# Performance work log

Measured on AMD Instinct MI355X. Metric: run time of the kernel, lower is better.

## Reference

```python
import jax, jax.numpy as jnp
import numpy as np

T = 16          # time_span
N = 128         # num_trajectory
D = 512         # embedding dim
TEMP = 0.1      # temperature
INF = 1000000000.0
M = 2 * N * T   # total rows of z (two views)


def setup_inputs() -> dict:
    key = jax.random.key(0)
    k1, k2 = jax.random.split(key)
    z = jax.random.normal(k1, (M, D), dtype=jnp.float32)
    done = jax.random.randint(k2, (T, N), 0, 2).astype(jnp.int32)  # [T, N] binary done flags
    return {"z": z, "done": done}


def _build_positive_mask(done):
    # done: [T, N] int -> transposed to [N, T] as in the torch code
    d = done.astype(jnp.float32).T  # [N, T]
    # Sequential rewrite loop is equivalent to:
    #   done_new[r,t] = 1 iff exists original done at p < t in row r AND orig done[r,t] == 0
    excl = jnp.cumsum(d, axis=1) - d  # exclusive cumsum along time
    d_new = jnp.where((excl > 0) & (d == 0), 1.0, 0.0)  # [N, T]
    done_vec = 1.0 - d_new.reshape(-1)  # [N*T]
    # block-diagonal temporal mask: same trajectory => 1
    traj = jnp.arange(N * T) // T
    block = (traj[:, None] == traj[None, :]).astype(jnp.float32)  # [NT, NT]
    done_mask = (done_vec[:, None] * done_vec[None, :]) * block
    done_mask = jnp.tile(done_mask, (2, 2))      # [M, M]
    temporal_mask = jnp.tile(block, (2, 2))      # [M, M]
    eye = jnp.eye(M, dtype=jnp.float32)
    positive_mask = (1.0 - done_mask) * (1.0 - temporal_mask) + eye
    return positive_mask, eye


def reference(z, done):
    positive_mask, eye = _build_positive_mask(done)
    # cosine similarity = normalize + GEMM (same math as broadcasted F.cosine_similarity)
    norms = jnp.maximum(jnp.linalg.norm(z, axis=-1, keepdims=True), 1e-8)
    zn = z / norms
    logits = (zn @ zn.T) / TEMP - eye * INF  # [M, M]
    log_probs = jax.nn.log_softmax(logits, axis=1)
    neg = 1.0 - positive_mask
    mean_log_prob = jnp.sum(neg * log_probs, axis=1) / jnp.sum(neg, axis=1)
    return -jnp.mean(mean_log_prob)
```

## Files before the change

kernel.cpp:

```cpp
#include <hip/hip_runtime.h>
#include <hip/hip_bf16.h>

typedef __bf16 bf16x8 __attribute__((ext_vector_type(8)));
typedef float f32x16 __attribute__((ext_vector_type(16)));
typedef unsigned int u32x4 __attribute__((ext_vector_type(4)));
typedef unsigned short u16;


__global__ void nrm_kernel(const float* __restrict__ z, u16* __restrict__ zn,
                           float* __restrict__ expsum) {
    int tid = threadIdx.x;
    int l = tid & 63, w = tid >> 6;
    int row = blockIdx.x * 4 + w;
    const float4* src = (const float4*)(z + row * 512);
    float4 v0 = src[l];
    float4 v1 = src[l + 64];
    float ss = v0.x * v0.x + v0.y * v0.y + v0.z * v0.z + v0.w * v0.w
             + v1.x * v1.x + v1.y * v1.y + v1.z * v1.z + v1.w * v1.w;
#pragma unroll
    for (int off = 32; off; off >>= 1) ss += __shfl_xor(ss, off, 64);
    float sc = 1.0f / fmaxf(sqrtf(ss), 1e-8f);
    __hip_bfloat16 b0[4], b1[4];
    b0[0] = __float2bfloat16(v0.x * sc); b0[1] = __float2bfloat16(v0.y * sc);
    b0[2] = __float2bfloat16(v0.z * sc); b0[3] = __float2bfloat16(v0.w * sc);
    b1[0] = __float2bfloat16(v1.x * sc); b1[1] = __float2bfloat16(v1.y * sc);
    b1[2] = __float2bfloat16(v1.z * sc); b1[3] = __float2bfloat16(v1.w * sc);
    uint2 p0, p1;
    __builtin_memcpy(&p0, b0, 8);
    __builtin_memcpy(&p1, b1, 8);
    ((uint2*)(zn + row * 512))[l] = p0;
    ((uint2*)(zn + row * 512))[l + 64] = p1;
    int gi = blockIdx.x * 256 + tid;
    if (gi < 4096) expsum[gi] = 0.f;
}

__global__ __launch_bounds__(256, 1) void gemm_kernel(const u16* __restrict__ zn,
                                                      float* __restrict__ expsum,
                                                      float* __restrict__ possum) {
    __shared__ u16 Bt[2][32 * 512];

    int tid = threadIdx.x;
    int wave = tid >> 6;
    int l = tid & 63;
    int m = l & 31, h = l >> 5;

    if (blockIdx.x >= 528) {
        if (tid < 64) {
            int g = blockIdx.x - 528;
            int grow = (m < 16) ? (g * 16 + m) : (2048 + g * 16 + (m - 16));
            const u32x4* src = (const u32x4*)(zn + grow * 512);
            f32x16 acc = {};
#pragma unroll
            for (int kc = 0; kc < 32; ++kc) {
                bf16x8 f = __builtin_bit_cast(bf16x8, src[h + 2 * kc]);
                acc = __builtin_amdgcn_mfma_f32_32x32x16_bf16(f, f, acc, 0, 0, 0);
            }
#pragma unroll
            for (int r = 0; r < 16; ++r) {
                int rrow = (r & 3) + 8 * (r >> 2) + 4 * h;
                float v = (rrow == m) ? 0.f : acc[r];
                v += __shfl_xor(v, 1, 64);
                v += __shfl_xor(v, 2, 64);
                v += __shfl_xor(v, 4, 64);
                v += __shfl_xor(v, 8, 64);
                v += __shfl_xor(v, 16, 64);
                if (m == 0) {
                    int gr = (rrow < 16) ? (g * 16 + rrow) : (2048 + g * 16 + (rrow - 16));
                    possum[gr] = v * 10.0f;
                }
            }
        }
        return;
    }

    int b = blockIdx.x;
    int ti = 0;
    while (b >= 32 - ti) { b -= 32 - ti; ++ti; }
    int tj = ti + b;

    int rowbase = ti * 128 + wave * 32;
    int colbase = tj * 128;
    bool diag = (ti == tj);

    u32x4 a[32];
    const u32x4* arow = (const u32x4*)(zn + (rowbase + m) * 512);
#pragma unroll
    for (int kc = 0; kc < 32; ++kc) a[kc] = arow[h + 2 * kc];

    float racc[16];
#pragma unroll
    for (int r = 0; r < 16; ++r) racc[r] = 0.f;
    float colacc[4] = {0.f, 0.f, 0.f, 0.f};

    int c = tid >> 3, g0 = tid & 7;
    int wbase = (g0 >> 1) * 1024 + (g0 & 1) * 512 + c * 16;
    const u32x4* zsrc = (const u32x4*)(zn + (colbase + c) * 512);

    u32x4 stg[8];
    {
#pragma unroll
        for (int i = 0; i < 8; ++i) stg[i] = zsrc[g0 + 8 * i];
        char* dst = (char*)Bt[0] + wbase;
#pragma unroll
        for (int i = 0; i < 8; ++i) *(u32x4*)(dst + i * 4096) = stg[i];
    }
    __syncthreads();

#pragma unroll
    for (int ct = 0; ct < 4; ++ct) {
        if (ct < 3) {
            const u32x4* nsrc = zsrc + (ct + 1) * 2048;
#pragma unroll
            for (int i = 0; i < 8; ++i) stg[i] = nsrc[g0 + 8 * i];
        }
        const char* rb = (const char*)Bt[ct & 1] + l * 16;
        f32x16 acc = {};
        __builtin_amdgcn_s_setprio(1);
#pragma unroll
        for (int kc = 0; kc < 32; ++kc) {
            bf16x8 bf = *(const bf16x8*)(rb + kc * 1024);
            acc = __builtin_amdgcn_mfma_f32_32x32x16_bf16(
                __builtin_bit_cast(bf16x8, a[kc]), bf, acc, 0, 0, 0);
        }
        __builtin_amdgcn_s_setprio(0);

        if (diag && ct == wave) {
#pragma unroll
            for (int r = 0; r < 16; ++r) {
                int rrow = (r & 3) + 8 * (r >> 2) + 4 * h;
                if (rrow != m) racc[r] += __builtin_exp2f(acc[r] * 14.426950408889634f);
            }
        } else {
            float csum = 0.f;
#pragma unroll
            for (int r = 0; r < 16; ++r) {
                float e = __builtin_exp2f(acc[r] * 14.426950408889634f);
                racc[r] += e;
                csum += e;
            }
            colacc[ct] += csum;
        }

        if (ct < 3) {
            char* dst = (char*)Bt[(ct + 1) & 1] + wbase;
#pragma unroll
            for (int i = 0; i < 8; ++i) *(u32x4*)(dst + i * 4096) = stg[i];
        }
        __syncthreads();
    }

#pragma unroll
    for (int r = 0; r < 16; ++r) {
        float v = racc[r];
        v += __shfl_xor(v, 1, 64);
        v += __shfl_xor(v, 2, 64);
        v += __shfl_xor(v, 4, 64);
        v += __shfl_xor(v, 8, 64);
        v += __shfl_xor(v, 16, 64);
        if (m == 0) {
            int rrow = (r & 3) + 8 * (r >> 2) + 4 * h;
            atomicAdd(&expsum[rowbase + rrow], v);
        }
    }

    if (!diag) {
        float* colred = (float*)Bt;
#pragma unroll
        for (int ct = 0; ct < 4; ++ct) {
            float v = colacc[ct] + __shfl_xor(colacc[ct], 32, 64);
            if (h == 0) colred[wave * 128 + ct * 32 + m] = v;
        }
        __syncthreads();
        if (tid < 128) {
            float s = colred[tid] + colred[128 + tid] + colred[256 + tid] + colred[384 + tid];
            atomicAdd(&expsum[colbase + tid], s);
        }
    }
}

__global__ void fin_kernel(const float* __restrict__ expsum,
                           const float* __restrict__ possum, float* __restrict__ out) {
    int tid = threadIdx.x;
    float s = 0.f;
    for (int i = tid; i < 4096; i += 1024)
        s += __logf(expsum[i]) - possum[i] * (1.0f / 31.0f);
#pragma unroll
    for (int off = 32; off; off >>= 1) s += __shfl_down(s, off, 64);
    __shared__ float red[16];
    if ((tid & 63) == 0) red[tid >> 6] = s;
    __syncthreads();
    if (tid == 0) {
        float t = 0.f;
#pragma unroll
        for (int i = 0; i < 16; ++i) t += red[i];
        out[0] = t * (1.0f / 4096.0f);
    }
}

extern "C" void kernel_launch(void* const* d_in, const int* in_sizes, int n_in,
                              void* d_out, int out_size, void* d_ws, size_t ws_size,
                              hipStream_t stream) {
    const float* z = (const float*)d_in[0];
    u16* zn = (u16*)d_ws;
    float* expsum = (float*)((char*)d_ws + (4u << 20));
    float* possum = expsum + 4096;
    float* out = (float*)d_out;

    nrm_kernel<<<1024, 256, 0, stream>>>(z, zn, expsum);
    gemm_kernel<<<656, 256, 0, stream>>>(zn, expsum, possum);
    fin_kernel<<<1, 1024, 0, stream>>>(expsum, possum, out);
}
```

Before: 108.6 us.

## Replace expsum atomics with per-tile partial buffer and two-stage final reduction

The GEMM kernel no longer atomically accumulates row exp-sums. Each tile instead writes its row and column partial sums into a 4096x32 buffer indexed by tile column or tile row. The final reduction becomes a 16-block kernel that sums each row's 32 partials, takes the log, and writes a per-block partial, followed by a tiny kernel that combines them. This removes atomic contention and the zeroing pass in the normalize kernel, and it also drops the s_setprio hints around the MFMA loop, at the cost of one extra kernel launch and a larger intermediate buffer.

```diff
diff --git a/kernel.cpp b/kernel.cpp
--- a/kernel.cpp
+++ b/kernel.cpp
@@ -7,8 +7,7 @@
 typedef unsigned short u16;
 
 
-__global__ void nrm_kernel(const float* __restrict__ z, u16* __restrict__ zn,
-                           float* __restrict__ expsum) {
+__global__ void nrm_kernel(const float* __restrict__ z, u16* __restrict__ zn) {
     int tid = threadIdx.x;
     int l = tid & 63, w = tid >> 6;
     int row = blockIdx.x * 4 + w;
@@ -30,12 +29,10 @@
     __builtin_memcpy(&p1, b1, 8);
     ((uint2*)(zn + row * 512))[l] = p0;
     ((uint2*)(zn + row * 512))[l + 64] = p1;
-    int gi = blockIdx.x * 256 + tid;
-    if (gi < 4096) expsum[gi] = 0.f;
 }
 
 __global__ __launch_bounds__(256, 1) void gemm_kernel(const u16* __restrict__ zn,
-                                                      float* __restrict__ expsum,
+                                                      float* __restrict__ merged,
                                                       float* __restrict__ possum) {
     __shared__ u16 Bt[2][32 * 512];
 
@@ -115,14 +112,12 @@
         }
         const char* rb = (const char*)Bt[ct & 1] + l * 16;
         f32x16 acc = {};
-        __builtin_amdgcn_s_setprio(1);
 #pragma unroll
         for (int kc = 0; kc < 32; ++kc) {
             bf16x8 bf = *(const bf16x8*)(rb + kc * 1024);
             acc = __builtin_amdgcn_mfma_f32_32x32x16_bf16(
                 __builtin_bit_cast(bf16x8, a[kc]), bf, acc, 0, 0, 0);
         }
-        __builtin_amdgcn_s_setprio(0);
 
         if (diag && ct == wave) {
 #pragma unroll
@@ -159,7 +154,7 @@
         v += __shfl_xor(v, 16, 64);
         if (m == 0) {
             int rrow = (r & 3) + 8 * (r >> 2) + 4 * h;
-            atomicAdd(&expsum[rowbase + rrow], v);
+            merged[(rowbase + rrow) * 32 + tj] = v;
         }
     }
 
@@ -173,28 +168,40 @@
         __syncthreads();
         if (tid < 128) {
             float s = colred[tid] + colred[128 + tid] + colred[256 + tid] + colred[384 + tid];
-            atomicAdd(&expsum[colbase + tid], s);
-        }
-    }
-}
-
-__global__ void fin_kernel(const float* __restrict__ expsum,
-                           const float* __restrict__ possum, float* __restrict__ out) {
+            merged[(colbase + tid) * 32 + ti] = s;
+        }
+    }
+}
+
+__global__ void finA_kernel(const float* __restrict__ merged,
+                            const float* __restrict__ possum,
+                            float* __restrict__ partial) {
     int tid = threadIdx.x;
+    int r = blockIdx.x * 256 + tid;
+    const float4* mrow = (const float4*)(merged + r * 32);
     float s = 0.f;
-    for (int i = tid; i < 4096; i += 1024)
-        s += __logf(expsum[i]) - possum[i] * (1.0f / 31.0f);
-#pragma unroll
-    for (int off = 32; off; off >>= 1) s += __shfl_down(s, off, 64);
-    __shared__ float red[16];
-    if ((tid & 63) == 0) red[tid >> 6] = s;
+#pragma unroll
+    for (int i = 0; i < 8; ++i) {
+        float4 v = mrow[i];
+        s += (v.x + v.y) + (v.z + v.w);
+    }
+    float loss = __logf(s) - possum[r] * (1.0f / 31.0f);
+#pragma unroll
+    for (int off = 32; off; off >>= 1) loss += __shfl_xor(loss, off, 64);
+    __shared__ float red[4];
+    if ((tid & 63) == 0) red[tid >> 6] = loss;
     __syncthreads();
-    if (tid == 0) {
-        float t = 0.f;
-#pragma unroll
-        for (int i = 0; i < 16; ++i) t += red[i];
-        out[0] = t * (1.0f / 4096.0f);
-    }
+    if (tid == 0) partial[blockIdx.x] = (red[0] + red[1]) + (red[2] + red[3]);
+}
+
+__global__ void finB_kernel(const float* __restrict__ partial, float* __restrict__ out) {
+    int l = threadIdx.x;
+    float v = (l < 16) ? partial[l] : 0.f;
+    v += __shfl_xor(v, 1, 64);
+    v += __shfl_xor(v, 2, 64);
+    v += __shfl_xor(v, 4, 64);
+    v += __shfl_xor(v, 8, 64);
+    if (l == 0) out[0] = v * (1.0f / 4096.0f);
 }
 
 extern "C" void kernel_launch(void* const* d_in, const int* in_sizes, int n_in,
@@ -202,11 +209,13 @@
                               hipStream_t stream) {
     const float* z = (const float*)d_in[0];
     u16* zn = (u16*)d_ws;
-    float* expsum = (float*)((char*)d_ws + (4u << 20));
-    float* possum = expsum + 4096;
+    float* merged = (float*)((char*)d_ws + (4u << 20));
+    float* possum = merged + 4096 * 32;
+    float* partial = possum + 4096;
     float* out = (float*)d_out;
 
-    nrm_kernel<<<1024, 256, 0, stream>>>(z, zn, expsum);
-    gemm_kernel<<<656, 256, 0, stream>>>(zn, expsum, possum);
-    fin_kernel<<<1, 1024, 0, stream>>>(expsum, possum, out);
-}
+    nrm_kernel<<<1024, 256, 0, stream>>>(z, zn);
+    gemm_kernel<<<656, 256, 0, stream>>>(zn, merged, possum);
+    finA_kernel<<<16, 256, 0, stream>>>(merged, possum, partial);
+    finB_kernel<<<1, 64, 0, stream>>>(partial, out);
+}
```

After: 108.8 us. Within noise of the previous version (+0.2%).
